# Optimization experiments

Measured on AMD Instinct MI355X. Metric: run time of the kernel, lower is better.

Reference implementation:

```python
import jax, jax.numpy as jnp
import numpy as np

B, S, D, H, MAX_OBJ, N_IMGS = 256, 256, 256, 4, 50, 32


def setup_inputs() -> dict:
    key = jax.random.key(0)
    ks = jax.random.split(key, 8)
    std = 1.0 / np.sqrt(D)
    mk = lambda k: (jax.random.normal(k, (D, D), jnp.float32) * std)
    return {
        "batch_seq": jax.random.normal(ks[0], (B, S, D), jnp.float32),
        "img_ids": jax.random.randint(ks[1], (B,), 0, N_IMGS, jnp.int32),
        "Wq": mk(ks[2]), "Wk": mk(ks[3]), "Wv": mk(ks[4]), "Wo": mk(ks[5]),
        "bq": jnp.zeros((D,), jnp.float32), "bk": jnp.zeros((D,), jnp.float32),
        "bv": jnp.zeros((D,), jnp.float32), "bo": jnp.zeros((D,), jnp.float32),
        "obj_emb": jax.random.normal(ks[6], (MAX_OBJ, D), jnp.float32) * 0.02,
        "scale": jnp.ones((1,), jnp.float32) * 0.2,
    }


def reference(batch_seq, img_ids, Wq, Wk, Wv, Wo, bq, bk, bv, bo, obj_emb, scale):
    Bn, Sn, Dn = batch_seq.shape
    dh = Dn // H
    idx = jnp.arange(Bn)
    same = img_ids[:, None] == img_ids[None, :]          # (B, B) group membership
    rank = jnp.sum(same & (idx[None, :] < idx[:, None]), axis=1)  # position within group
    gsize = jnp.sum(same, axis=1)                         # group size per item

    # enhanced features: add rank-indexed object embedding (broadcast over seq)
    enh = batch_seq + scale * obj_emb[rank][:, None, :]   # (B, S, D)

    # MHA over the seq dimension, batched over B (eval mode, no dropout)
    q = (enh @ Wq + bq).reshape(Bn, Sn, H, dh)
    k = (enh @ Wk + bk).reshape(Bn, Sn, H, dh)
    v = (enh @ Wv + bv).reshape(Bn, Sn, H, dh)
    scores = jnp.einsum("bqhd,bkhd->bhqk", q, k) / float(np.sqrt(dh))
    attn = jax.nn.softmax(scores, axis=-1)
    ctx = jnp.einsum("bhqk,bkhd->bqhd", attn, v).reshape(Bn, Sn, Dn)
    att_out = ctx @ Wo + bo

    # residual; items in singleton groups are passed through unchanged
    return jnp.where((gsize > 1)[:, None, None], batch_seq + att_out, batch_seq)
```

## Files before the change

### kernel.cpp

```cpp
#include <hip/hip_runtime.h>

typedef __bf16 bf16x8 __attribute__((ext_vector_type(8)));
typedef float f32x4 __attribute__((ext_vector_type(4)));
typedef ushort u16x8 __attribute__((ext_vector_type(8)));

__device__ __forceinline__ float bf2f(ushort u) {
    union { unsigned int i; float f; } v; v.i = ((unsigned int)u) << 16; return v.f;
}
__device__ __forceinline__ ushort f2bf(float f) {
    union { float f; unsigned int i; } v; v.f = f;
    unsigned int i = v.i;
    return (ushort)((i + 0x7FFFu + ((i >> 16) & 1u)) >> 16);
}
__device__ __forceinline__ unsigned int addmul_bf2(unsigned int xs, unsigned int es, float sc) {
    float f0 = bf2f((ushort)(xs & 0xffffu)) + sc * bf2f((ushort)(es & 0xffffu));
    float f1 = bf2f((ushort)(xs >> 16))     + sc * bf2f((ushort)(es >> 16));
    return (unsigned int)f2bf(f0) | (((unsigned int)f2bf(f1)) << 16);
}
__device__ __forceinline__ void cp16(void* lds, const void* g) {
    __builtin_amdgcn_global_load_lds(
        (const __attribute__((address_space(1))) unsigned int*)g,
        (__attribute__((address_space(3))) unsigned int*)lds, 16, 0, 0);
}

__global__ __launch_bounds__(256) void sniff_kernel(
    const unsigned int* __restrict__ bs_words, int* __restrict__ flag)
{
    const int t = threadIdx.x;
    int hit = 0;
    for (int i = 0; i < 64; ++i) {
        unsigned int w = bs_words[t * 64 + i];
        unsigned int e0 = (w >> 7)  & 0xffu;
        unsigned int e1 = (w >> 23) & 0xffu;
        if (e0 > 150u || e1 > 150u) hit = 1;
    }
    __shared__ int s;
    if (t == 0) s = 0;
    __syncthreads();
    if (hit) atomicOr(&s, 1);
    __syncthreads();
    if (t == 0) *flag = s;
}

__global__ __launch_bounds__(256) void prep_kernel(
    const int* __restrict__ flag,
    const void* __restrict__ Wq, const void* __restrict__ Wk,
    const void* __restrict__ Wv, const void* __restrict__ Wo,
    const void* __restrict__ c0, const void* __restrict__ c1,
    const void* __restrict__ c2, const void* __restrict__ c3,
    const void* __restrict__ c4, const void* __restrict__ scale_in,
    int* __restrict__ rank, int* __restrict__ gsize,
    ushort* __restrict__ Wqkv_t, ushort* __restrict__ Wo_t,
    float* __restrict__ bqkv_f, float* __restrict__ bo_f,
    float* __restrict__ scale_f)
{
    const int blk = blockIdx.x;
    const int t = threadIdx.x;
    const bool is_f32 = (*flag != 0);
    if (blk < 256) {
        const int k = blk;
        ushort q, kk, vv, oo;
        if (is_f32) {
            q  = f2bf(((const float*)Wq)[k * 256 + t]);
            kk = f2bf(((const float*)Wk)[k * 256 + t]);
            vv = f2bf(((const float*)Wv)[k * 256 + t]);
            oo = f2bf(((const float*)Wo)[k * 256 + t]);
        } else {
            q  = ((const ushort*)Wq)[k * 256 + t];
            kk = ((const ushort*)Wk)[k * 256 + t];
            vv = ((const ushort*)Wv)[k * 256 + t];
            oo = ((const ushort*)Wo)[k * 256 + t];
        }
        Wqkv_t[(size_t)t * 256 + k]         = q;
        Wqkv_t[(size_t)(256 + t) * 256 + k] = kk;
        Wqkv_t[(size_t)(512 + t) * 256 + k] = vv;
        Wo_t[(size_t)t * 256 + k]           = oo;
    } else {
        const void* cands[5] = {c0, c1, c2, c3, c4};
        __shared__ int cstat[5];
        if (t < 5) cstat[t] = 0;
        __syncthreads();
        #pragma unroll
        for (int c = 0; c < 5; ++c) {
            unsigned int wv = ((const unsigned int*)cands[c])[t];
            int fl = ((wv != 0u) ? 1 : 0) | ((wv >= 32u) ? 2 : 0);
            if (fl) atomicOr(&cstat[c], fl);
        }
        __syncthreads();
        int sel = 0;
        #pragma unroll
        for (int c = 4; c >= 0; --c)
            if (cstat[c] == 1) sel = c;
        const int* ids = (const int*)cands[sel];
        int bp[4];
        { int n = 0;
          #pragma unroll
          for (int c = 0; c < 5; ++c) if (c != sel) bp[n++] = c; }

        const int b = t;
        const int my = ids[b];
        int r = 0, g = 0;
        for (int j = 0; j < 256; ++j) {
            bool same = (ids[j] == my);
            r += (same && (j < b)) ? 1 : 0;
            g += same ? 1 : 0;
        }
        rank[b]  = (r > 49) ? 49 : r;
        gsize[b] = g;

        float vq, vk, vv2, vo2;
        if (is_f32) {
            vq  = ((const float*)cands[bp[0]])[t];
            vk  = ((const float*)cands[bp[1]])[t];
            vv2 = ((const float*)cands[bp[2]])[t];
            vo2 = ((const float*)cands[bp[3]])[t];
            if (t == 0) *scale_f = ((const float*)scale_in)[0];
        } else {
            vq  = bf2f(((const ushort*)cands[bp[0]])[t]);
            vk  = bf2f(((const ushort*)cands[bp[1]])[t]);
            vv2 = bf2f(((const ushort*)cands[bp[2]])[t]);
            vo2 = bf2f(((const ushort*)cands[bp[3]])[t]);
            if (t == 0) *scale_f = bf2f(((const ushort*)scale_in)[0]);
        }
        bqkv_f[t]       = vq;
        bqkv_f[256 + t] = vk;
        bqkv_f[512 + t] = vv2;
        bo_f[t]         = vo2;
    }
}

__global__ __launch_bounds__(256) void enh_kernel(
    const int* __restrict__ flag,
    const void* __restrict__ bs, const void* __restrict__ obj_emb,
    const float* __restrict__ scale_f, const int* __restrict__ rank,
    ushort* __restrict__ enh)
{
    const int idx = blockIdx.x * 256 + threadIdx.x;
    const int e0 = idx * 8;
    const int b = e0 >> 16;
    const int col = e0 & 255;
    const int rk = rank[b];
    const float sc = *scale_f;
    if (*flag != 0) {
        const float* bsf = (const float*)bs + e0;
        const float* ef  = (const float*)obj_emb + rk * 256 + col;
        float4 x0 = *(const float4*)bsf, x1 = *(const float4*)(bsf + 4);
        float4 ev0 = *(const float4*)ef, ev1 = *(const float4*)(ef + 4);
        u16x8 o;
        o[0] = f2bf(x0.x + sc * ev0.x); o[1] = f2bf(x0.y + sc * ev0.y);
        o[2] = f2bf(x0.z + sc * ev0.z); o[3] = f2bf(x0.w + sc * ev0.w);
        o[4] = f2bf(x1.x + sc * ev1.x); o[5] = f2bf(x1.y + sc * ev1.y);
        o[6] = f2bf(x1.z + sc * ev1.z); o[7] = f2bf(x1.w + sc * ev1.w);
        *(u16x8*)(enh + e0) = o;
    } else {
        uint4 x = *(const uint4*)((const ushort*)bs + e0);
        uint4 e = *(const uint4*)((const ushort*)obj_emb + rk * 256 + col);
        uint4 o;
        o.x = addmul_bf2(x.x, e.x, sc);
        o.y = addmul_bf2(x.y, e.y, sc);
        o.z = addmul_bf2(x.z, e.z, sc);
        o.w = addmul_bf2(x.w, e.w, sc);
        *(uint4*)(enh + e0) = o;
    }
}

__global__ __launch_bounds__(256, 2) void qkv_kernel(
    const ushort* __restrict__ enh, const ushort* __restrict__ Wqkv_t,
    const float* __restrict__ bqkv_f,
    ushort* __restrict__ Qg, ushort* __restrict__ Kg, ushort* __restrict__ Vt)
{
    __shared__ __attribute__((aligned(16))) ushort A_lds[64 * 32];
    __shared__ __attribute__((aligned(16))) ushort B_lds[256 * 32];

    const int m0 = blockIdx.y * 64;
    const int n0 = blockIdx.x * 256;
    const int b  = m0 >> 8;
    const int tid = threadIdx.x;
    const int w = tid >> 6, l = tid & 63, quad = l >> 4, l15 = l & 15;

    f32x4 acc[4][4];
    #pragma unroll
    for (int i = 0; i < 4; ++i)
        #pragma unroll
        for (int j = 0; j < 4; ++j) { f32x4 z = {0.f,0.f,0.f,0.f}; acc[i][j] = z; }

    for (int k0 = 0; k0 < 256; k0 += 32) {
        cp16(&A_lds[tid * 8],
             enh + ((size_t)(m0 + (tid >> 2)) << 8) + k0 + (tid & 3) * 8);
        #pragma unroll
        for (int i = 0; i < 4; ++i) {
            const int f = tid + i * 256;
            cp16(&B_lds[f * 8],
                 Wqkv_t + ((size_t)(n0 + (f >> 2)) << 8) + k0 + (f & 3) * 8);
        }
        __syncthreads();
        bf16x8 a[4], bb[4];
        #pragma unroll
        for (int mt = 0; mt < 4; ++mt)
            a[mt] = *(const bf16x8*)&A_lds[(mt * 16 + l15) * 32 + quad * 8];
        #pragma unroll
        for (int nt = 0; nt < 4; ++nt)
            bb[nt] = *(const bf16x8*)&B_lds[(w * 64 + nt * 16 + l15) * 32 + quad * 8];
        #pragma unroll
        for (int mt = 0; mt < 4; ++mt)
            #pragma unroll
            for (int nt = 0; nt < 4; ++nt)
                acc[mt][nt] = __builtin_amdgcn_mfma_f32_16x16x32_bf16(
                    a[mt], bb[nt], acc[mt][nt], 0, 0, 0);
        __syncthreads();
    }

    #pragma unroll
    for (int nt = 0; nt < 4; ++nt) {
        const int n_g = n0 + w * 64 + nt * 16 + l15;
        const int seg = n_g >> 8;
        const int within = n_g & 255;
        const int h = within >> 6, d = within & 63;
        const float bias = bqkv_f[n_g];
        const size_t bh = (size_t)(b * 4 + h);
        #pragma unroll
        for (int mt = 0; mt < 4; ++mt) {
            const int sbase = (m0 & 255) + mt * 16 + quad * 4;
            if (seg == 2) {
                ushort pk[4];
                #pragma unroll
                for (int r = 0; r < 4; ++r) pk[r] = f2bf(acc[mt][nt][r] + bias);
                *(ushort4*)(Vt + (bh * 64 + d) * 256 + sbase) =
                    make_ushort4(pk[0], pk[1], pk[2], pk[3]);
            } else if (seg == 0) {
                #pragma unroll
                for (int r = 0; r < 4; ++r)
                    Qg[(bh * 256 + sbase + r) * 64 + d] =
                        f2bf((acc[mt][nt][r] + bias) * 0.125f);
            } else {
                #pragma unroll
                for (int r = 0; r < 4; ++r)
                    Kg[(bh * 256 + sbase + r) * 64 + d] = f2bf(acc[mt][nt][r] + bias);
            }
        }
    }
}

__global__ __launch_bounds__(256, 2) void attn_kernel(
    const ushort* __restrict__ Qg, const ushort* __restrict__ Kg,
    const ushort* __restrict__ Vt, ushort* __restrict__ ctx)
{
    __shared__ __attribute__((aligned(16))) ushort Pl[4][64 * 72];
    const int bh = blockIdx.x;
    const int b = bh >> 2, h = bh & 3;
    const int tid = threadIdx.x;
    const int w = tid >> 6, l = tid & 63, quad = l >> 4, l15 = l & 15;

    const ushort* Qb = Qg + (size_t)bh * 256 * 64;
    const ushort* Kb = Kg + (size_t)bh * 256 * 64;
    const ushort* Vb = Vt + (size_t)bh * 64 * 256;

    bf16x8 qf[4][2];
    #pragma unroll
    for (int mt = 0; mt < 4; ++mt)
        #pragma unroll
        for (int ks = 0; ks < 2; ++ks) {
            int s = w * 64 + mt * 16 + l15;
            qf[mt][ks] = *(const bf16x8*)(Qb + (size_t)s * 64 + ks * 32 + quad * 8);
        }

    f32x4 O[4][4];
    float m_run[4][4], l_run[4][4];
    #pragma unroll
    for (int mt = 0; mt < 4; ++mt) {
        #pragma unroll
        for (int dt = 0; dt < 4; ++dt) { f32x4 z = {0.f,0.f,0.f,0.f}; O[mt][dt] = z; }
        #pragma unroll
        for (int r = 0; r < 4; ++r) { m_run[mt][r] = -1e30f; l_run[mt][r] = 0.f; }
    }

    for (int c = 0; c < 4; ++c) {
        bf16x8 vf[2][4];
        #pragma unroll
        for (int ks = 0; ks < 2; ++ks)
            #pragma unroll
            for (int dt = 0; dt < 4; ++dt)
                vf[ks][dt] = *(const bf16x8*)(Vb + (size_t)(dt * 16 + l15) * 256 +
                                              c * 64 + ks * 32 + quad * 8);

        f32x4 sacc[4][4];
        #pragma unroll
        for (int mt = 0; mt < 4; ++mt)
            #pragma unroll
            for (int nt = 0; nt < 4; ++nt) { f32x4 z = {0.f,0.f,0.f,0.f}; sacc[mt][nt] = z; }
        #pragma unroll
        for (int ks = 0; ks < 2; ++ks) {
            bf16x8 kf[4];
            #pragma unroll
            for (int nt = 0; nt < 4; ++nt) {
                int key = c * 64 + nt * 16 + l15;
                kf[nt] = *(const bf16x8*)(Kb + (size_t)key * 64 + ks * 32 + quad * 8);
            }
            #pragma unroll
            for (int mt = 0; mt < 4; ++mt)
                #pragma unroll
                for (int nt = 0; nt < 4; ++nt)
                    sacc[mt][nt] = __builtin_amdgcn_mfma_f32_16x16x32_bf16(
                        qf[mt][ks], kf[nt], sacc[mt][nt], 0, 0, 0);
        }

        #pragma unroll
        for (int mt = 0; mt < 4; ++mt) {
            f32x4 mx = sacc[mt][0];
            #pragma unroll
            for (int nt = 1; nt < 4; ++nt)
                #pragma unroll
                for (int r = 0; r < 4; ++r) mx[r] = fmaxf(mx[r], sacc[mt][nt][r]);
            #pragma unroll
            for (int r = 0; r < 4; ++r) {
                float v = mx[r];
                v = fmaxf(v, __shfl_xor(v, 1));
                v = fmaxf(v, __shfl_xor(v, 2));
                v = fmaxf(v, __shfl_xor(v, 4));
                v = fmaxf(v, __shfl_xor(v, 8));
                mx[r] = v;
            }
            float rs[4];
            #pragma unroll
            for (int r = 0; r < 4; ++r) {
                float nm = fmaxf(m_run[mt][r], mx[r]);
                float alpha = __expf(m_run[mt][r] - nm);
                m_run[mt][r] = nm;
                l_run[mt][r] *= alpha;
                float sum = 0.f;
                #pragma unroll
                for (int nt = 0; nt < 4; ++nt) {
                    float p = __expf(sacc[mt][nt][r] - nm);
                    sacc[mt][nt][r] = p;
                    sum += p;
                }
                rs[r] = sum;
                #pragma unroll
                for (int dt = 0; dt < 4; ++dt) O[mt][dt][r] *= alpha;
            }
            #pragma unroll
            for (int r = 0; r < 4; ++r) {
                float v = rs[r];
                v += __shfl_xor(v, 1);
                v += __shfl_xor(v, 2);
                v += __shfl_xor(v, 4);
                v += __shfl_xor(v, 8);
                l_run[mt][r] += v;
            }
            #pragma unroll
            for (int nt = 0; nt < 4; ++nt)
                #pragma unroll
                for (int r = 0; r < 4; ++r)
                    Pl[w][(mt * 16 + quad * 4 + r) * 72 + nt * 16 + l15] =
                        f2bf(sacc[mt][nt][r]);
        }

        #pragma unroll
        for (int ks = 0; ks < 2; ++ks) {
            bf16x8 pf[4];
            #pragma unroll
            for (int mt = 0; mt < 4; ++mt)
                pf[mt] = *(const bf16x8*)&Pl[w][(mt * 16 + l15) * 72 + ks * 32 + quad * 8];
            #pragma unroll
            for (int mt = 0; mt < 4; ++mt)
                #pragma unroll
                for (int dt = 0; dt < 4; ++dt)
                    O[mt][dt] = __builtin_amdgcn_mfma_f32_16x16x32_bf16(
                        pf[mt], vf[ks][dt], O[mt][dt], 0, 0, 0);
        }
    }

    #pragma unroll
    for (int mt = 0; mt < 4; ++mt) {
        #pragma unroll
        for (int r = 0; r < 4; ++r) {
            float inv = 1.0f / l_run[mt][r];
            const int s = w * 64 + mt * 16 + quad * 4 + r;
            const size_t base = ((size_t)(b * 256 + s)) * 256 + h * 64;
            #pragma unroll
            for (int dt = 0; dt < 4; ++dt)
                ctx[base + dt * 16 + l15] = f2bf(O[mt][dt][r] * inv);
        }
    }
}

__global__ __launch_bounds__(256, 2) void out_kernel(
    const int* __restrict__ flag,
    const ushort* __restrict__ ctx, const ushort* __restrict__ Wo_t,
    const float* __restrict__ bo_f, const void* __restrict__ bs,
    const int* __restrict__ gsize, void* __restrict__ outv)
{
    __shared__ __attribute__((aligned(16))) ushort A_lds[64 * 32];
    __shared__ __attribute__((aligned(16))) ushort B_lds[256 * 32];

    const int m0 = blockIdx.x * 64;
    const int tid = threadIdx.x;
    const int w = tid >> 6, l = tid & 63, quad = l >> 4, l15 = l & 15;
    const int b = m0 >> 8;
    const bool pass = (gsize[b] <= 1);
    const bool is_f32 = (*flag != 0);

    f32x4 acc[4][4];
    #pragma unroll
    for (int i = 0; i < 4; ++i)
        #pragma unroll
        for (int j = 0; j < 4; ++j) { f32x4 z = {0.f,0.f,0.f,0.f}; acc[i][j] = z; }

    for (int k0 = 0; k0 < 256; k0 += 32) {
        cp16(&A_lds[tid * 8],
             ctx + ((size_t)(m0 + (tid >> 2)) << 8) + k0 + (tid & 3) * 8);
        #pragma unroll
        for (int i = 0; i < 4; ++i) {
            const int f = tid + i * 256;
            cp16(&B_lds[f * 8],
                 Wo_t + ((size_t)(f >> 2) << 8) + k0 + (f & 3) * 8);
        }
        __syncthreads();
        bf16x8 a[4], bb[4];
        #pragma unroll
        for (int mt = 0; mt < 4; ++mt)
            a[mt] = *(const bf16x8*)&A_lds[(mt * 16 + l15) * 32 + quad * 8];
        #pragma unroll
        for (int nt = 0; nt < 4; ++nt)
            bb[nt] = *(const bf16x8*)&B_lds[(w * 64 + nt * 16 + l15) * 32 + quad * 8];
        #pragma unroll
        for (int mt = 0; mt < 4; ++mt)
            #pragma unroll
            for (int nt = 0; nt < 4; ++nt)
                acc[mt][nt] = __builtin_amdgcn_mfma_f32_16x16x32_bf16(
                    a[mt], bb[nt], acc[mt][nt], 0, 0, 0);
        __syncthreads();
    }

    #pragma unroll
    for (int nt = 0; nt < 4; ++nt) {
        const int n = w * 64 + nt * 16 + l15;
        const float bias = bo_f[n];
        #pragma unroll
        for (int mt = 0; mt < 4; ++mt)
            #pragma unroll
            for (int r = 0; r < 4; ++r) {
                int token = m0 + mt * 16 + quad * 4 + r;
                size_t idx = (((size_t)token) << 8) + n;
                float base = is_f32 ? ((const float*)bs)[idx]
                                    : bf2f(((const ushort*)bs)[idx]);
                float v = pass ? base : (base + acc[mt][nt][r] + bias);
                if (is_f32) ((float*)outv)[idx] = v;
                else        ((ushort*)outv)[idx] = f2bf(v);
            }
    }
}

extern "C" void kernel_launch(void* const* d_in, const int* in_sizes, int n_in,
                              void* d_out, int out_size, void* d_ws, size_t ws_size,
                              hipStream_t stream)
{
    int bs_i = -1, obj_i = -1, sc_i = -1;
    int w_i[4] = {2, 3, 4, 5}; int nw = 0;
    int c_i[5] = {1, 6, 7, 8, 9}; int nc = 0;
    for (int i = 0; i < n_in; ++i) {
        int s = in_sizes[i];
        if      (s == 16777216) bs_i = i;
        else if (s == 65536)  { if (nw < 4) w_i[nw] = i; ++nw; }
        else if (s == 12800)    obj_i = i;
        else if (s == 1)        sc_i = i;
        else if (s == 256)    { if (nc < 5) c_i[nc] = i; ++nc; }
    }
    if (bs_i < 0 || obj_i < 0 || sc_i < 0 || nw != 4 || nc != 5) {
        bs_i = 0; obj_i = 10; sc_i = 11;
        w_i[0] = 2; w_i[1] = 3; w_i[2] = 4; w_i[3] = 5;
        c_i[0] = 1; c_i[1] = 6; c_i[2] = 7; c_i[3] = 8; c_i[4] = 9;
    }
    const void* bs    = d_in[bs_i];
    const void* Wq    = d_in[w_i[0]];
    const void* Wk    = d_in[w_i[1]];
    const void* Wv    = d_in[w_i[2]];
    const void* Wo    = d_in[w_i[3]];
    const void* obj   = d_in[obj_i];
    const void* scale = d_in[sc_i];

    char* ws = (char*)d_ws;
    int*    flag    = (int*)ws;
    int*    rank    = (int*)(ws + 1024);
    int*    gsize   = (int*)(ws + 2048);
    float*  scale_f = (float*)(ws + 3072);
    float*  bqkv_f  = (float*)(ws + 4096);
    float*  bo_f    = (float*)(ws + 8192);
    ushort* Wqkv_t  = (ushort*)(ws + 16384);
    ushort* Wo_t    = (ushort*)(ws + 409600);
    ushort* enh     = (ushort*)(ws + ((size_t)1  << 20));
    ushort* ctx     = (ushort*)(ws + ((size_t)33 << 20));
    ushort* Vt      = (ushort*)(ws + ((size_t)65 << 20));

    ushort* Qg = (ushort*)d_out;
    ushort* Kg = Qg + 16777216;

    hipLaunchKernelGGL(sniff_kernel, dim3(1), dim3(256), 0, stream,
                       (const unsigned int*)bs, flag);
    hipLaunchKernelGGL(prep_kernel, dim3(257), dim3(256), 0, stream,
                       flag, Wq, Wk, Wv, Wo,
                       d_in[c_i[0]], d_in[c_i[1]], d_in[c_i[2]],
                       d_in[c_i[3]], d_in[c_i[4]], scale,
                       rank, gsize, Wqkv_t, Wo_t, bqkv_f, bo_f, scale_f);
    hipLaunchKernelGGL(enh_kernel, dim3(8192), dim3(256), 0, stream,
                       flag, bs, obj, scale_f, rank, enh);
    hipLaunchKernelGGL(qkv_kernel, dim3(3, 1024), dim3(256), 0, stream,
                       enh, Wqkv_t, bqkv_f, Qg, Kg, Vt);
    hipLaunchKernelGGL(attn_kernel, dim3(1024), dim3(256), 0, stream,
                       Qg, Kg, Vt, ctx);
    hipLaunchKernelGGL(out_kernel, dim3(1024), dim3(256), 0, stream,
                       flag, ctx, Wo_t, bo_f, bs, gsize, d_out);
}
```

Measured before the change: 338.4 us.

## Stage GEMM epilogues through LDS for coalesced vector stores; drop global_load_lds

```diff
diff --git a/kernel.cpp b/kernel.cpp
--- a/kernel.cpp
+++ b/kernel.cpp
@@ -16,11 +16,6 @@
     float f0 = bf2f((ushort)(xs & 0xffffu)) + sc * bf2f((ushort)(es & 0xffffu));
     float f1 = bf2f((ushort)(xs >> 16))     + sc * bf2f((ushort)(es >> 16));
     return (unsigned int)f2bf(f0) | (((unsigned int)f2bf(f1)) << 16);
-}
-__device__ __forceinline__ void cp16(void* lds, const void* g) {
-    __builtin_amdgcn_global_load_lds(
-        (const __attribute__((address_space(1))) unsigned int*)g,
-        (__attribute__((address_space(3))) unsigned int*)lds, 16, 0, 0);
 }
 
 __global__ __launch_bounds__(256) void sniff_kernel(
@@ -171,9 +166,11 @@
 {
     __shared__ __attribute__((aligned(16))) ushort A_lds[64 * 32];
     __shared__ __attribute__((aligned(16))) ushort B_lds[256 * 32];
+    __shared__ __attribute__((aligned(16))) ushort Tw[4][64 * 72];
 
     const int m0 = blockIdx.y * 64;
-    const int n0 = blockIdx.x * 256;
+    const int seg = blockIdx.x;
+    const int n0 = seg * 256;
     const int b  = m0 >> 8;
     const int tid = threadIdx.x;
     const int w = tid >> 6, l = tid & 63, quad = l >> 4, l15 = l & 15;
@@ -184,14 +181,16 @@
         #pragma unroll
         for (int j = 0; j < 4; ++j) { f32x4 z = {0.f,0.f,0.f,0.f}; acc[i][j] = z; }
 
+    const int arow = tid >> 2, ako = (tid & 3) * 8;
     for (int k0 = 0; k0 < 256; k0 += 32) {
-        cp16(&A_lds[tid * 8],
-             enh + ((size_t)(m0 + (tid >> 2)) << 8) + k0 + (tid & 3) * 8);
+        *(uint4*)&A_lds[arow * 32 + ako] =
+            *(const uint4*)(enh + (((size_t)(m0 + arow)) << 8) + k0 + ako);
         #pragma unroll
         for (int i = 0; i < 4; ++i) {
-            const int f = tid + i * 256;
-            cp16(&B_lds[f * 8],
-                 Wqkv_t + ((size_t)(n0 + (f >> 2)) << 8) + k0 + (f & 3) * 8);
+            int f = tid + i * 256;
+            int n = f >> 2, ko = (f & 3) * 8;
+            *(uint4*)&B_lds[n * 32 + ko] =
+                *(const uint4*)(Wqkv_t + (((size_t)(n0 + n)) << 8) + k0 + ko);
         }
         __syncthreads();
         bf16x8 a[4], bb[4];
@@ -210,32 +209,44 @@
         __syncthreads();
     }
 
-    #pragma unroll
-    for (int nt = 0; nt < 4; ++nt) {
-        const int n_g = n0 + w * 64 + nt * 16 + l15;
-        const int seg = n_g >> 8;
-        const int within = n_g & 255;
-        const int h = within >> 6, d = within & 63;
-        const float bias = bqkv_f[n_g];
-        const size_t bh = (size_t)(b * 4 + h);
-        #pragma unroll
-        for (int mt = 0; mt < 4; ++mt) {
-            const int sbase = (m0 & 255) + mt * 16 + quad * 4;
-            if (seg == 2) {
+    if (seg < 2) {
+        const float qs = (seg == 0) ? 0.125f : 1.0f;
+        #pragma unroll
+        for (int nt = 0; nt < 4; ++nt) {
+            const float bias = bqkv_f[seg * 256 + w * 64 + nt * 16 + l15];
+            #pragma unroll
+            for (int mt = 0; mt < 4; ++mt)
+                #pragma unroll
+                for (int r = 0; r < 4; ++r)
+                    Tw[w][(mt * 16 + quad * 4 + r) * 72 + nt * 16 + l15] =
+                        f2bf((acc[mt][nt][r] + bias) * qs);
+        }
+        ushort* dst = (seg == 0) ? Qg : Kg;
+        const size_t bh = (size_t)(b * 4 + w);
+        const int sb = m0 & 255;
+        #pragma unroll
+        for (int i = 0; i < 8; ++i) {
+            const int chunk = i * 64 + l;
+            const int row = chunk >> 3, dch = chunk & 7;
+            u16x8 v = *(const u16x8*)&Tw[w][row * 72 + dch * 8];
+            *(u16x8*)(dst + (bh * 256 + sb + row) * 64 + dch * 8) = v;
+        }
+    } else {
+        #pragma unroll
+        for (int nt = 0; nt < 4; ++nt) {
+            const int n_g = n0 + w * 64 + nt * 16 + l15;
+            const int within = n_g & 255;
+            const int h = within >> 6, d = within & 63;
+            const float bias = bqkv_f[n_g];
+            const size_t bh = (size_t)(b * 4 + h);
+            #pragma unroll
+            for (int mt = 0; mt < 4; ++mt) {
+                const int sbase = (m0 & 255) + mt * 16 + quad * 4;
                 ushort pk[4];
                 #pragma unroll
                 for (int r = 0; r < 4; ++r) pk[r] = f2bf(acc[mt][nt][r] + bias);
                 *(ushort4*)(Vt + (bh * 64 + d) * 256 + sbase) =
                     make_ushort4(pk[0], pk[1], pk[2], pk[3]);
-            } else if (seg == 0) {
-                #pragma unroll
-                for (int r = 0; r < 4; ++r)
-                    Qg[(bh * 256 + sbase + r) * 64 + d] =
-                        f2bf((acc[mt][nt][r] + bias) * 0.125f);
-            } else {
-                #pragma unroll
-                for (int r = 0; r < 4; ++r)
-                    Kg[(bh * 256 + sbase + r) * 64 + d] = f2bf(acc[mt][nt][r] + bias);
             }
         }
     }
@@ -371,16 +382,21 @@
     }
 
     #pragma unroll
-    for (int mt = 0; mt < 4; ++mt) {
+    for (int mt = 0; mt < 4; ++mt)
         #pragma unroll
         for (int r = 0; r < 4; ++r) {
             float inv = 1.0f / l_run[mt][r];
-            const int s = w * 64 + mt * 16 + quad * 4 + r;
-            const size_t base = ((size_t)(b * 256 + s)) * 256 + h * 64;
             #pragma unroll
             for (int dt = 0; dt < 4; ++dt)
-                ctx[base + dt * 16 + l15] = f2bf(O[mt][dt][r] * inv);
-        }
+                Pl[w][(mt * 16 + quad * 4 + r) * 72 + dt * 16 + l15] =
+                    f2bf(O[mt][dt][r] * inv);
+        }
+    #pragma unroll
+    for (int i = 0; i < 8; ++i) {
+        const int chunk = i * 64 + l;
+        const int row = chunk >> 3, dch = chunk & 7;
+        u16x8 v = *(const u16x8*)&Pl[w][row * 72 + dch * 8];
+        *(u16x8*)(ctx + ((size_t)(b * 256 + w * 64 + row)) * 256 + h * 64 + dch * 8) = v;
     }
 }
 
@@ -392,6 +408,7 @@
 {
     __shared__ __attribute__((aligned(16))) ushort A_lds[64 * 32];
     __shared__ __attribute__((aligned(16))) ushort B_lds[256 * 32];
+    __shared__ __attribute__((aligned(16))) float  Tf[4][16 * 68];
 
     const int m0 = blockIdx.x * 64;
     const int tid = threadIdx.x;
@@ -406,14 +423,16 @@
         #pragma unroll
         for (int j = 0; j < 4; ++j) { f32x4 z = {0.f,0.f,0.f,0.f}; acc[i][j] = z; }
 
+    const int arow = tid >> 2, ako = (tid & 3) * 8;
     for (int k0 = 0; k0 < 256; k0 += 32) {
-        cp16(&A_lds[tid * 8],
-             ctx + ((size_t)(m0 + (tid >> 2)) << 8) + k0 + (tid & 3) * 8);
+        *(uint4*)&A_lds[arow * 32 + ako] =
+            *(const uint4*)(ctx + (((size_t)(m0 + arow)) << 8) + k0 + ako);
         #pragma unroll
         for (int i = 0; i < 4; ++i) {
-            const int f = tid + i * 256;
-            cp16(&B_lds[f * 8],
-                 Wo_t + ((size_t)(f >> 2) << 8) + k0 + (f & 3) * 8);
+            int f = tid + i * 256;
+            int n = f >> 2, ko = (f & 3) * 8;
+            *(uint4*)&B_lds[n * 32 + ko] =
+                *(const uint4*)(Wo_t + (((size_t)n) << 8) + k0 + ko);
         }
         __syncthreads();
         bf16x8 a[4], bb[4];
@@ -432,22 +451,39 @@
         __syncthreads();
     }
 
-    #pragma unroll
-    for (int nt = 0; nt < 4; ++nt) {
-        const int n = w * 64 + nt * 16 + l15;
-        const float bias = bo_f[n];
-        #pragma unroll
-        for (int mt = 0; mt < 4; ++mt)
-            #pragma unroll
-            for (int r = 0; r < 4; ++r) {
-                int token = m0 + mt * 16 + quad * 4 + r;
-                size_t idx = (((size_t)token) << 8) + n;
-                float base = is_f32 ? ((const float*)bs)[idx]
-                                    : bf2f(((const ushort*)bs)[idx]);
-                float v = pass ? base : (base + acc[mt][nt][r] + bias);
-                if (is_f32) ((float*)outv)[idx] = v;
-                else        ((ushort*)outv)[idx] = f2bf(v);
+    for (int mt = 0; mt < 4; ++mt) {
+        #pragma unroll
+        for (int nt = 0; nt < 4; ++nt) {
+            const float bias = bo_f[w * 64 + nt * 16 + l15];
+            #pragma unroll
+            for (int r = 0; r < 4; ++r)
+                Tf[w][(quad * 4 + r) * 68 + nt * 16 + l15] = acc[mt][nt][r] + bias;
+        }
+        #pragma unroll
+        for (int i = 0; i < 4; ++i) {
+            const int chunk = i * 64 + l;
+            const int row = chunk >> 4, c4 = chunk & 15;
+            f32x4 v = *(const f32x4*)&Tf[w][row * 68 + c4 * 4];
+            const int token = m0 + mt * 16 + row;
+            const size_t idx = (((size_t)token) << 8) + w * 64 + c4 * 4;
+            if (is_f32) {
+                float4 base = *(const float4*)((const float*)bs + idx);
+                float4 o;
+                o.x = pass ? base.x : base.x + v[0];
+                o.y = pass ? base.y : base.y + v[1];
+                o.z = pass ? base.z : base.z + v[2];
+                o.w = pass ? base.w : base.w + v[3];
+                *(float4*)((float*)outv + idx) = o;
+            } else {
+                ushort4 b4 = *(const ushort4*)((const ushort*)bs + idx);
+                ushort4 o;
+                o.x = pass ? b4.x : f2bf(bf2f(b4.x) + v[0]);
+                o.y = pass ? b4.y : f2bf(bf2f(b4.y) + v[1]);
+                o.z = pass ? b4.z : f2bf(bf2f(b4.z) + v[2]);
+                o.w = pass ? b4.w : f2bf(bf2f(b4.w) + v[3]);
+                *(ushort4*)((ushort*)outv + idx) = o;
             }
+        }
     }
 }
 
```

Result: faster. 308.4 us (-8.9%).
